# Kernel tuning notes

Measured on AMD Instinct MI355X. Metric: run time of the kernel, lower is better.

The kernel has to match this reference:

```python
import jax, jax.numpy as jnp
import numpy as np

B, N, D, E = 4, 16384, 128, 1048576  # batch, nodes/graph, hidden, total edges


def setup_inputs() -> dict:
    key = jax.random.key(0)
    k0, k1, k2, k3, k4, k5, k6 = jax.random.split(key, 7)
    x = jax.random.normal(k0, (B, N, D), dtype=jnp.float32)
    W = jax.random.normal(k1, (D, D), dtype=jnp.float32) * 0.05  # 'random_normal' init
    b = jax.random.normal(k2, (D,), dtype=jnp.float32) * 0.05
    edge_b = jax.random.randint(k3, (E,), 0, B, dtype=jnp.int32)
    edge_row = jax.random.randint(k4, (E,), 0, N, dtype=jnp.int32)
    edge_col = jax.random.randint(k5, (E,), 0, N, dtype=jnp.int32)
    edge_vals = jax.random.uniform(k6, (E,), dtype=jnp.float32)
    return {"x": x, "W": W, "b": b, "edge_b": edge_b, "edge_row": edge_row,
            "edge_col": edge_col, "edge_vals": edge_vals, "k": 2}


def reference(x, W, b, edge_b, edge_row, edge_col, edge_vals, k):
    # adj is a batched sparse [B, N, N]; edges stored as (batch, row, col, val) COO.
    seg_row = edge_b * N + edge_row  # flattened destination id in [0, B*N)
    # in_degrees = sum_j |adj[b, i, j]|
    deg = jax.ops.segment_sum(jnp.abs(edge_vals), seg_row, num_segments=B * N)
    deg = deg.reshape(B, N)
    norm = jnp.power(deg + 1e-6, -0.5)[..., None]          # [B, N, 1]
    norm_k = jnp.power(norm, k)                             # computed but unused (faithful to source)
    support = jnp.einsum('bnd,de->bne', x, W)               # x @ W
    y = (support * norm).reshape(B * N, D)                  # pre-normalized features
    # SpMM: out[b, i] = sum_{(b,i,j)} adj_val * y[b, j]
    msgs = y[edge_b * N + edge_col] * edge_vals[:, None]    # [E, D] gather + scale
    agg = jax.ops.segment_sum(msgs, seg_row, num_segments=B * N).reshape(B, N, D)
    return jax.nn.relu(agg * norm + b)
```

## Files before the change

kernel.cpp:

```cpp
#include <hip/hip_runtime.h>
#include <stdint.h>

#define B_ 4
#define N_ 16384
#define D_ 128
#define E_ 1048576
#define BN_ 65536
#define NBKT 256
#define NBLK 256
#define CAP  6144

typedef __attribute__((ext_vector_type(8))) short short8;
typedef __attribute__((ext_vector_type(4))) float floatx4;

static constexpr size_t OFF_Y      = 0;
static constexpr size_t OFF_PACK2  = 16777216;
static constexpr size_t OFF_GBKT   = OFF_PACK2 + 12582912;
static constexpr size_t OFF_CURSOR = OFF_GBKT + 1024;
static constexpr size_t OFF_NORM   = OFF_CURSOR + 262144;
static constexpr size_t OFF_WH     = OFF_NORM + 262144;
static constexpr size_t OFF_WL     = OFF_WH + 32768;

__device__ __forceinline__ uint32_t rne16(uint32_t u) {
    return (u + 0x7FFFu + ((u >> 16) & 1u)) >> 16;
}
__device__ __forceinline__ void bf16split(float f, uint16_t& h, uint16_t& l) {
    uint32_t hb = rne16(__float_as_uint(f));
    h = (uint16_t)hb;
    float r = f - __uint_as_float(hb << 16);
    l = (uint16_t)rne16(__float_as_uint(r));
}

__global__ __launch_bounds__(1024) void k_scatter(const int* __restrict__ eb,
                                                  const int* __restrict__ er,
                                                  const int* __restrict__ ec,
                                                  const float* __restrict__ ev,
                                                  const float* __restrict__ Wg,
                                                  uint32_t* __restrict__ gbkt,
                                                  uint2* __restrict__ pack1,
                                                  uint16_t* __restrict__ WhG,
                                                  uint16_t* __restrict__ WlG) {
    __shared__ uint2    ed[4096];
    __shared__ uint32_t h[NBKT];
    int t = threadIdx.x;
    if (t < NBKT) h[t] = 0;
    if (blockIdx.x < 16) {
        int g = blockIdx.x * 1024 + t;
        float w = Wg[g];
        uint16_t hh, ll;
        bf16split(w, hh, ll);
        int k = g >> 7, n = g & 127;
        int o = ((k >> 3) * 128 + n) * 8 + (k & 7);
        WhG[o] = hh;
        WlG[o] = ll;
    }
    __syncthreads();
    int vbase = blockIdx.x * 1024 + t;
    int4   b4 = ((const int4*)eb)[vbase];
    int4   r4 = ((const int4*)er)[vbase];
    int4   c4 = ((const int4*)ec)[vbase];
    float4 v4 = ((const float4*)ev)[vbase];
    uint32_t k0 = (uint32_t)(b4.x * N_ + r4.x);
    uint32_t k1 = (uint32_t)(b4.y * N_ + r4.y);
    uint32_t k2 = (uint32_t)(b4.z * N_ + r4.z);
    uint32_t k3 = (uint32_t)(b4.w * N_ + r4.w);
    ed[t * 4 + 0] = make_uint2((k0 << 14) | (uint32_t)c4.x, __float_as_uint(v4.x));
    ed[t * 4 + 1] = make_uint2((k1 << 14) | (uint32_t)c4.y, __float_as_uint(v4.y));
    ed[t * 4 + 2] = make_uint2((k2 << 14) | (uint32_t)c4.z, __float_as_uint(v4.z));
    ed[t * 4 + 3] = make_uint2((k3 << 14) | (uint32_t)c4.w, __float_as_uint(v4.w));
    atomicAdd(&h[k0 >> 8], 1u);
    atomicAdd(&h[k1 >> 8], 1u);
    atomicAdd(&h[k2 >> 8], 1u);
    atomicAdd(&h[k3 >> 8], 1u);
    __syncthreads();
    if (t < NBKT) {
        uint32_t c = h[t];
        uint32_t base = c ? atomicAdd(&gbkt[t], c) : 0u;
        h[t] = base;
    }
    __syncthreads();
#pragma unroll
    for (int i = 0; i < 4; ++i) {
        uint2 en = ed[t * 4 + i];
        uint32_t bkt = en.x >> 22;
        uint32_t off = atomicAdd(&h[bkt], 1u);
        pack1[(size_t)bkt * CAP + off] = make_uint2(en.x & 0x3FFFFFu, en.y);
    }
}

__global__ __launch_bounds__(1024) void k_build(const uint32_t* __restrict__ gbkt,
                                                const uint2* __restrict__ pack1,
                                                uint2* __restrict__ pack2,
                                                uint32_t* __restrict__ cursor,
                                                float* __restrict__ norm) {
    __shared__ uint32_t cnt[NBKT];
    __shared__ float    dsum[NBKT];
    __shared__ uint32_t scn[NBKT];
    __shared__ uint32_t rcur[NBKT];
    int t = threadIdx.x;
    int bkt = blockIdx.x;
    uint32_t bstart = (uint32_t)bkt * CAP;
    uint32_t bend = bstart + gbkt[bkt];
    if (t < NBKT) { cnt[t] = 0; dsum[t] = 0.f; }
    __syncthreads();
    for (uint32_t i = bstart + t; i < bend; i += 1024) {
        uint2 p = pack1[i];
        uint32_t nl = p.x >> 14;
        atomicAdd(&cnt[nl], 1u);
        atomicAdd(&dsum[nl], fabsf(__uint_as_float(p.y)));
    }
    __syncthreads();
    if (t < NBKT) scn[t] = cnt[t];
    __syncthreads();
    for (int off = 1; off < NBKT; off <<= 1) {
        uint32_t a = 0;
        if (t < NBKT && t >= off) a = scn[t - off];
        __syncthreads();
        if (t < NBKT) scn[t] += a;
        __syncthreads();
    }
    if (t < NBKT) {
        uint32_t incl = scn[t];
        uint32_t excl = incl - cnt[t];
        rcur[t] = bstart + excl;
        cursor[bkt * NBKT + t] = bstart + incl;
        norm[bkt * NBKT + t] = rsqrtf(dsum[t] + 1e-6f);
    }
    __syncthreads();
    uint32_t colbase = (uint32_t)(bkt >> 6) * N_;
    for (uint32_t i = bstart + t; i < bend; i += 1024) {
        uint2 p = pack1[i];
        uint32_t nl = p.x >> 14;
        uint32_t pos = atomicAdd(&rcur[nl], 1u);
        pack2[pos] = make_uint2(colbase + (p.x & 0x3FFFu), p.y);
    }
}

__global__ __launch_bounds__(256) void k_matmul_mfma(const float* __restrict__ x,
                                                     const uint16_t* __restrict__ WhG,
                                                     const uint16_t* __restrict__ WlG,
                                                     const float* __restrict__ norm,
                                                     uint32_t* __restrict__ ybf) {
    __shared__ short WhS[16384];
    __shared__ short WlS[16384];
    __shared__ short XhS[4096];
    __shared__ short XlS[4096];
    __shared__ float normS[32];
    int tid = threadIdx.x;
    int row0 = blockIdx.x * 32;

    {
        const uint4* whg = (const uint4*)WhG;
        const uint4* wlg = (const uint4*)WlG;
        uint4* whs = (uint4*)WhS;
        uint4* wls = (uint4*)WlS;
#pragma unroll
        for (int i = 0; i < 8; ++i) {
            whs[i * 256 + tid] = whg[i * 256 + tid];
            wls[i * 256 + tid] = wlg[i * 256 + tid];
        }
    }
#pragma unroll
    for (int cc = 0; cc < 2; ++cc) {
        int c = cc * 256 + tid;
        int m = c & 31, kk = c >> 5;
        const float4* xp = (const float4*)(x + (size_t)(row0 + m) * D_ + kk * 8);
        float4 f0 = xp[0], f1 = xp[1];
        union { short8 v; uint16_t s[8]; } uh, ul;
        bf16split(f0.x, uh.s[0], ul.s[0]); bf16split(f0.y, uh.s[1], ul.s[1]);
        bf16split(f0.z, uh.s[2], ul.s[2]); bf16split(f0.w, uh.s[3], ul.s[3]);
        bf16split(f1.x, uh.s[4], ul.s[4]); bf16split(f1.y, uh.s[5], ul.s[5]);
        bf16split(f1.z, uh.s[6], ul.s[6]); bf16split(f1.w, uh.s[7], ul.s[7]);
        ((short8*)XhS)[c] = uh.v;
        ((short8*)XlS)[c] = ul.v;
    }
    if (tid < 32) normS[tid] = norm[row0 + tid];
    __syncthreads();

    int lane = tid & 63;
    int wv = tid >> 6;
    int quad = lane >> 4;
    int l15 = lane & 15;
    int wcol0 = wv * 32;
    floatx4 acc[2][2] = {};
    const short8* Xh8 = (const short8*)XhS;
    const short8* Xl8 = (const short8*)XlS;
    const short8* Wh8 = (const short8*)WhS;
    const short8* Wl8 = (const short8*)WlS;
#pragma unroll
    for (int ks = 0; ks < 4; ++ks) {
        int kkq = ks * 4 + quad;
        short8 ah0 = Xh8[kkq * 32 + l15];
        short8 ah1 = Xh8[kkq * 32 + 16 + l15];
        short8 al0 = Xl8[kkq * 32 + l15];
        short8 al1 = Xl8[kkq * 32 + 16 + l15];
        short8 bh0 = Wh8[kkq * 128 + wcol0 + l15];
        short8 bh1 = Wh8[kkq * 128 + wcol0 + 16 + l15];
        short8 bl0 = Wl8[kkq * 128 + wcol0 + l15];
        short8 bl1 = Wl8[kkq * 128 + wcol0 + 16 + l15];
        acc[0][0] = __builtin_amdgcn_mfma_f32_16x16x32_bf16(ah0, bh0, acc[0][0], 0, 0, 0);
        acc[0][1] = __builtin_amdgcn_mfma_f32_16x16x32_bf16(ah0, bh1, acc[0][1], 0, 0, 0);
        acc[1][0] = __builtin_amdgcn_mfma_f32_16x16x32_bf16(ah1, bh0, acc[1][0], 0, 0, 0);
        acc[1][1] = __builtin_amdgcn_mfma_f32_16x16x32_bf16(ah1, bh1, acc[1][1], 0, 0, 0);
        acc[0][0] = __builtin_amdgcn_mfma_f32_16x16x32_bf16(ah0, bl0, acc[0][0], 0, 0, 0);
        acc[0][1] = __builtin_amdgcn_mfma_f32_16x16x32_bf16(ah0, bl1, acc[0][1], 0, 0, 0);
        acc[1][0] = __builtin_amdgcn_mfma_f32_16x16x32_bf16(ah1, bl0, acc[1][0], 0, 0, 0);
        acc[1][1] = __builtin_amdgcn_mfma_f32_16x16x32_bf16(ah1, bl1, acc[1][1], 0, 0, 0);
        acc[0][0] = __builtin_amdgcn_mfma_f32_16x16x32_bf16(al0, bh0, acc[0][0], 0, 0, 0);
        acc[0][1] = __builtin_amdgcn_mfma_f32_16x16x32_bf16(al0, bh1, acc[0][1], 0, 0, 0);
        acc[1][0] = __builtin_amdgcn_mfma_f32_16x16x32_bf16(al1, bh0, acc[1][0], 0, 0, 0);
        acc[1][1] = __builtin_amdgcn_mfma_f32_16x16x32_bf16(al1, bh1, acc[1][1], 0, 0, 0);
    }

#pragma unroll
    for (int rt = 0; rt < 2; ++rt) {
#pragma unroll
        for (int ct = 0; ct < 2; ++ct) {
            floatx4 v = acc[rt][ct];
            int rbase = rt * 16 + quad * 4;
            int cp = (wcol0 + ct * 16) / 2 + (l15 >> 1);
#pragma unroll
            for (int r = 0; r < 4; ++r) {
                float mine = v[r] * normS[rbase + r];
                float oth = __shfl_xor(mine, 1, 64);
                uint32_t a = __float_as_uint((lane & 1) ? oth : mine);
                uint32_t b = __float_as_uint((lane & 1) ? mine : oth);
                uint32_t packed = rne16(a) | (rne16(b) << 16);
                bool doit = ((lane & 1) == 0) ? (r < 2) : (r >= 2);
                if (doit)
                    ybf[(size_t)(row0 + rbase + r) * 64 + cp] = packed;
            }
        }
    }
}

__device__ __forceinline__ void fma8(float* acc, float v, uint4 u) {
    acc[0] = fmaf(v, __uint_as_float(u.x << 16), acc[0]);
    acc[1] = fmaf(v, __uint_as_float(u.x & 0xFFFF0000u), acc[1]);
    acc[2] = fmaf(v, __uint_as_float(u.y << 16), acc[2]);
    acc[3] = fmaf(v, __uint_as_float(u.y & 0xFFFF0000u), acc[3]);
    acc[4] = fmaf(v, __uint_as_float(u.z << 16), acc[4]);
    acc[5] = fmaf(v, __uint_as_float(u.z & 0xFFFF0000u), acc[5]);
    acc[6] = fmaf(v, __uint_as_float(u.w << 16), acc[6]);
    acc[7] = fmaf(v, __uint_as_float(u.w & 0xFFFF0000u), acc[7]);
}

__global__ __launch_bounds__(256) void k_spmm(const uint32_t* __restrict__ cursor,
                                              const uint2* __restrict__ pack,
                                              const uint4* __restrict__ y4,
                                              const float* __restrict__ norm,
                                              const float* __restrict__ bias,
                                              float* __restrict__ out) {
    int blk = blockIdx.x;
    int xcd = blk & 7;
    int j = blk >> 3;
    int nodeblk = (xcd & 3) * 4096 + (xcd >> 2) * 2048 + j;
    int node = nodeblk * 4 + (threadIdx.x >> 6);
    int lane = threadIdx.x & 63;
    int esub = lane >> 4;
    int chunk = lane & 15;
    int nl = node & 255;
    uint32_t end = cursor[node];
    uint32_t start = (nl == 0) ? (uint32_t)(node >> 8) * CAP : cursor[node - 1];
    float acc[8] = {0.f,0.f,0.f,0.f,0.f,0.f,0.f,0.f};
    uint32_t e = start;
    for (; e + 16 <= end; e += 16) {
        uint2 pa = pack[e + 0 + esub];
        uint2 pb = pack[e + 4 + esub];
        uint2 pc = pack[e + 8 + esub];
        uint2 pd = pack[e + 12 + esub];
        uint4 ua = y4[(size_t)pa.x * 16 + chunk];
        uint4 ub = y4[(size_t)pb.x * 16 + chunk];
        uint4 uc = y4[(size_t)pc.x * 16 + chunk];
        uint4 ud = y4[(size_t)pd.x * 16 + chunk];
        fma8(acc, __uint_as_float(pa.y), ua);
        fma8(acc, __uint_as_float(pb.y), ub);
        fma8(acc, __uint_as_float(pc.y), uc);
        fma8(acc, __uint_as_float(pd.y), ud);
    }
    for (; e + 4 <= end; e += 4) {
        uint2 p = pack[e + esub];
        uint4 u = y4[(size_t)p.x * 16 + chunk];
        fma8(acc, __uint_as_float(p.y), u);
    }
    if (e < end) {
        uint32_t idx = e + esub;
        bool act = idx < end;
        uint2 p = pack[act ? idx : (end - 1)];
        uint4 u = y4[(size_t)p.x * 16 + chunk];
        float v = act ? __uint_as_float(p.y) : 0.f;
        fma8(acc, v, u);
    }
#pragma unroll
    for (int i = 0; i < 8; ++i) {
        acc[i] += __shfl_xor(acc[i], 16, 64);
        acc[i] += __shfl_xor(acc[i], 32, 64);
    }
    if (esub < 2) {
        float nm = norm[node];
        float4 bb = ((const float4*)bias)[chunk * 2 + esub];
        float4 o;
        o.x = fmaxf(fmaf(acc[esub * 4 + 0], nm, bb.x), 0.f);
        o.y = fmaxf(fmaf(acc[esub * 4 + 1], nm, bb.y), 0.f);
        o.z = fmaxf(fmaf(acc[esub * 4 + 2], nm, bb.z), 0.f);
        o.w = fmaxf(fmaf(acc[esub * 4 + 3], nm, bb.w), 0.f);
        ((float4*)out)[(size_t)node * 32 + chunk * 2 + esub] = o;
    }
}

extern "C" void kernel_launch(void* const* d_in, const int* in_sizes, int n_in,
                              void* d_out, int out_size, void* d_ws, size_t ws_size,
                              hipStream_t stream) {
    const float* x  = (const float*)d_in[0];
    const float* W  = (const float*)d_in[1];
    const float* bi = (const float*)d_in[2];
    const int* eb   = (const int*)d_in[3];
    const int* er   = (const int*)d_in[4];
    const int* ec   = (const int*)d_in[5];
    const float* ev = (const float*)d_in[6];
    float* out = (float*)d_out;

    char* ws = (char*)d_ws;
    uint32_t* ybf    = (uint32_t*)(ws + OFF_Y);
    uint2*    pack1  = (uint2*)(ws + OFF_Y);
    uint2*    pack2  = (uint2*)(ws + OFF_PACK2);
    uint32_t* gbkt   = (uint32_t*)(ws + OFF_GBKT);
    uint32_t* cursor = (uint32_t*)(ws + OFF_CURSOR);
    float*    norm   = (float*)(ws + OFF_NORM);
    uint16_t* WhG    = (uint16_t*)(ws + OFF_WH);
    uint16_t* WlG    = (uint16_t*)(ws + OFF_WL);

    hipMemsetAsync(gbkt, 0, NBKT * sizeof(uint32_t), stream);
    k_scatter<<<NBLK, 1024, 0, stream>>>(eb, er, ec, ev, W, gbkt, pack1, WhG, WlG);
    k_build  <<<NBKT, 1024, 0, stream>>>(gbkt, pack1, pack2, cursor, norm);
    k_matmul_mfma<<<BN_ / 32, 256, 0, stream>>>(x, WhG, WlG, norm, ybf);
    k_spmm   <<<BN_ / 4, 256, 0, stream>>>(cursor, pack2, (const uint4*)ybf, norm, bi, out);
}
```

Before: 183.7 us.

## Fuse per-bucket row sort into SpMM kernel via shared memory

The row-sorting of edges moves from a separate build kernel into the SpMM kernel. Each 1024-thread block loads one bucket into LDS, counting-sorts it by local row, then has each wave process 16 rows. This removes the global pack2 and cursor arrays and their extra write/read pass. The build kernel shrinks to a degree-only kernel. In exchange, SpMM runs with only 256 large blocks and heavy LDS use, which lowers latency hiding for the random gathers.

```diff
diff --git a/kernel.cpp b/kernel.cpp
--- a/kernel.cpp
+++ b/kernel.cpp
@@ -14,10 +14,9 @@
 typedef __attribute__((ext_vector_type(4))) float floatx4;
 
 static constexpr size_t OFF_Y      = 0;
-static constexpr size_t OFF_PACK2  = 16777216;
-static constexpr size_t OFF_GBKT   = OFF_PACK2 + 12582912;
-static constexpr size_t OFF_CURSOR = OFF_GBKT + 1024;
-static constexpr size_t OFF_NORM   = OFF_CURSOR + 262144;
+static constexpr size_t OFF_PACK1  = 16777216;
+static constexpr size_t OFF_GBKT   = OFF_PACK1 + 12582912;
+static constexpr size_t OFF_NORM   = OFF_GBKT + 1024;
 static constexpr size_t OFF_WH     = OFF_NORM + 262144;
 static constexpr size_t OFF_WL     = OFF_WH + 32768;
 
@@ -88,52 +87,22 @@
     }
 }
 
-__global__ __launch_bounds__(1024) void k_build(const uint32_t* __restrict__ gbkt,
-                                                const uint2* __restrict__ pack1,
-                                                uint2* __restrict__ pack2,
-                                                uint32_t* __restrict__ cursor,
-                                                float* __restrict__ norm) {
-    __shared__ uint32_t cnt[NBKT];
-    __shared__ float    dsum[NBKT];
-    __shared__ uint32_t scn[NBKT];
-    __shared__ uint32_t rcur[NBKT];
+__global__ __launch_bounds__(1024) void k_deg(const uint32_t* __restrict__ gbkt,
+                                              const uint2* __restrict__ pack1,
+                                              float* __restrict__ norm) {
+    __shared__ float dsum[NBKT];
     int t = threadIdx.x;
     int bkt = blockIdx.x;
-    uint32_t bstart = (uint32_t)bkt * CAP;
-    uint32_t bend = bstart + gbkt[bkt];
-    if (t < NBKT) { cnt[t] = 0; dsum[t] = 0.f; }
-    __syncthreads();
-    for (uint32_t i = bstart + t; i < bend; i += 1024) {
-        uint2 p = pack1[i];
-        uint32_t nl = p.x >> 14;
-        atomicAdd(&cnt[nl], 1u);
-        atomicAdd(&dsum[nl], fabsf(__uint_as_float(p.y)));
-    }
-    __syncthreads();
-    if (t < NBKT) scn[t] = cnt[t];
-    __syncthreads();
-    for (int off = 1; off < NBKT; off <<= 1) {
-        uint32_t a = 0;
-        if (t < NBKT && t >= off) a = scn[t - off];
-        __syncthreads();
-        if (t < NBKT) scn[t] += a;
-        __syncthreads();
-    }
-    if (t < NBKT) {
-        uint32_t incl = scn[t];
-        uint32_t excl = incl - cnt[t];
-        rcur[t] = bstart + excl;
-        cursor[bkt * NBKT + t] = bstart + incl;
-        norm[bkt * NBKT + t] = rsqrtf(dsum[t] + 1e-6f);
-    }
-    __syncthreads();
-    uint32_t colbase = (uint32_t)(bkt >> 6) * N_;
-    for (uint32_t i = bstart + t; i < bend; i += 1024) {
-        uint2 p = pack1[i];
-        uint32_t nl = p.x >> 14;
-        uint32_t pos = atomicAdd(&rcur[nl], 1u);
-        pack2[pos] = make_uint2(colbase + (p.x & 0x3FFFu), p.y);
-    }
+    if (t < NBKT) dsum[t] = 0.f;
+    __syncthreads();
+    uint32_t cnt = gbkt[bkt];
+    size_t bstart = (size_t)bkt * CAP;
+    for (uint32_t i = t; i < cnt; i += 1024) {
+        uint2 p = pack1[bstart + i];
+        atomicAdd(&dsum[p.x >> 14], fabsf(__uint_as_float(p.y)));
+    }
+    __syncthreads();
+    if (t < NBKT) norm[bkt * NBKT + t] = rsqrtf(dsum[t] + 1e-6f);
 }
 
 __global__ __launch_bounds__(256) void k_matmul_mfma(const float* __restrict__ x,
@@ -245,66 +214,97 @@
     acc[7] = fmaf(v, __uint_as_float(u.w & 0xFFFF0000u), acc[7]);
 }
 
-__global__ __launch_bounds__(256) void k_spmm(const uint32_t* __restrict__ cursor,
-                                              const uint2* __restrict__ pack,
-                                              const uint4* __restrict__ y4,
-                                              const float* __restrict__ norm,
-                                              const float* __restrict__ bias,
-                                              float* __restrict__ out) {
+__global__ __launch_bounds__(1024) void k_spmm(const uint32_t* __restrict__ gbkt,
+                                               const uint2* __restrict__ pack1,
+                                               const uint4* __restrict__ y4,
+                                               const float* __restrict__ norm,
+                                               const float* __restrict__ bias,
+                                               float* __restrict__ out) {
+    __shared__ uint2    raw[CAP];
+    __shared__ uint2    srt[CAP];
+    __shared__ uint32_t cnt[NBKT];
+    __shared__ uint32_t scn[NBKT];
+    __shared__ uint32_t rcur[NBKT];
+    int t = threadIdx.x;
     int blk = blockIdx.x;
     int xcd = blk & 7;
-    int j = blk >> 3;
-    int nodeblk = (xcd & 3) * 4096 + (xcd >> 2) * 2048 + j;
-    int node = nodeblk * 4 + (threadIdx.x >> 6);
-    int lane = threadIdx.x & 63;
+    int bkt = ((xcd & 3) << 6) | ((xcd >> 2) << 5) | (blk >> 3);
+    if (t < NBKT) cnt[t] = 0;
+    __syncthreads();
+    uint32_t n = gbkt[bkt];
+    size_t base = (size_t)bkt * CAP;
+    for (uint32_t i = t; i < n; i += 1024) {
+        uint2 p = pack1[base + i];
+        raw[i] = p;
+        atomicAdd(&cnt[p.x >> 14], 1u);
+    }
+    __syncthreads();
+    if (t < NBKT) scn[t] = cnt[t];
+    __syncthreads();
+    for (int off = 1; off < NBKT; off <<= 1) {
+        uint32_t a = 0;
+        if (t < NBKT && t >= off) a = scn[t - off];
+        __syncthreads();
+        if (t < NBKT) scn[t] += a;
+        __syncthreads();
+    }
+    if (t < NBKT) rcur[t] = scn[t] - cnt[t];
+    __syncthreads();
+    for (uint32_t i = t; i < n; i += 1024) {
+        uint2 p = raw[i];
+        uint32_t pos = atomicAdd(&rcur[p.x >> 14], 1u);
+        srt[pos] = p;
+    }
+    __syncthreads();
+
+    int wv = t >> 6;
+    int lane = t & 63;
     int esub = lane >> 4;
     int chunk = lane & 15;
-    int nl = node & 255;
-    uint32_t end = cursor[node];
-    uint32_t start = (nl == 0) ? (uint32_t)(node >> 8) * CAP : cursor[node - 1];
-    float acc[8] = {0.f,0.f,0.f,0.f,0.f,0.f,0.f,0.f};
-    uint32_t e = start;
-    for (; e + 16 <= end; e += 16) {
-        uint2 pa = pack[e + 0 + esub];
-        uint2 pb = pack[e + 4 + esub];
-        uint2 pc = pack[e + 8 + esub];
-        uint2 pd = pack[e + 12 + esub];
-        uint4 ua = y4[(size_t)pa.x * 16 + chunk];
-        uint4 ub = y4[(size_t)pb.x * 16 + chunk];
-        uint4 uc = y4[(size_t)pc.x * 16 + chunk];
-        uint4 ud = y4[(size_t)pd.x * 16 + chunk];
-        fma8(acc, __uint_as_float(pa.y), ua);
-        fma8(acc, __uint_as_float(pb.y), ub);
-        fma8(acc, __uint_as_float(pc.y), uc);
-        fma8(acc, __uint_as_float(pd.y), ud);
-    }
-    for (; e + 4 <= end; e += 4) {
-        uint2 p = pack[e + esub];
-        uint4 u = y4[(size_t)p.x * 16 + chunk];
-        fma8(acc, __uint_as_float(p.y), u);
-    }
-    if (e < end) {
-        uint32_t idx = e + esub;
-        bool act = idx < end;
-        uint2 p = pack[act ? idx : (end - 1)];
-        uint4 u = y4[(size_t)p.x * 16 + chunk];
-        float v = act ? __uint_as_float(p.y) : 0.f;
-        fma8(acc, v, u);
-    }
-#pragma unroll
-    for (int i = 0; i < 8; ++i) {
-        acc[i] += __shfl_xor(acc[i], 16, 64);
-        acc[i] += __shfl_xor(acc[i], 32, 64);
-    }
-    if (esub < 2) {
-        float nm = norm[node];
-        float4 bb = ((const float4*)bias)[chunk * 2 + esub];
-        float4 o;
-        o.x = fmaxf(fmaf(acc[esub * 4 + 0], nm, bb.x), 0.f);
-        o.y = fmaxf(fmaf(acc[esub * 4 + 1], nm, bb.y), 0.f);
-        o.z = fmaxf(fmaf(acc[esub * 4 + 2], nm, bb.z), 0.f);
-        o.w = fmaxf(fmaf(acc[esub * 4 + 3], nm, bb.w), 0.f);
-        ((float4*)out)[(size_t)node * 32 + chunk * 2 + esub] = o;
+    uint32_t colbase = (uint32_t)(bkt >> 6) << 14;
+#pragma unroll 1
+    for (int i = 0; i < 16; ++i) {
+        int nl = wv * 16 + i;
+        uint32_t end = scn[nl];
+        uint32_t e = end - cnt[nl];
+        float acc[8] = {0.f,0.f,0.f,0.f,0.f,0.f,0.f,0.f};
+        for (; e + 8 <= end; e += 8) {
+            uint2 p0 = srt[e + esub];
+            uint2 p1 = srt[e + 4 + esub];
+            uint4 u0 = y4[(size_t)(colbase | (p0.x & 0x3FFFu)) * 16 + chunk];
+            uint4 u1 = y4[(size_t)(colbase | (p1.x & 0x3FFFu)) * 16 + chunk];
+            fma8(acc, __uint_as_float(p0.y), u0);
+            fma8(acc, __uint_as_float(p1.y), u1);
+        }
+        for (; e + 4 <= end; e += 4) {
+            uint2 p = srt[e + esub];
+            uint4 u = y4[(size_t)(colbase | (p.x & 0x3FFFu)) * 16 + chunk];
+            fma8(acc, __uint_as_float(p.y), u);
+        }
+        if (e < end) {
+            uint32_t idx = e + esub;
+            bool act = idx < end;
+            uint2 p = srt[act ? idx : (end - 1)];
+            uint4 u = y4[(size_t)(colbase | (p.x & 0x3FFFu)) * 16 + chunk];
+            float v = act ? __uint_as_float(p.y) : 0.f;
+            fma8(acc, v, u);
+        }
+#pragma unroll
+        for (int j = 0; j < 8; ++j) {
+            acc[j] += __shfl_xor(acc[j], 16, 64);
+            acc[j] += __shfl_xor(acc[j], 32, 64);
+        }
+        if (esub < 2) {
+            int node = bkt * NBKT + nl;
+            float nm = norm[node];
+            float4 bb = ((const float4*)bias)[chunk * 2 + esub];
+            float4 o;
+            o.x = fmaxf(fmaf(acc[esub * 4 + 0], nm, bb.x), 0.f);
+            o.y = fmaxf(fmaf(acc[esub * 4 + 1], nm, bb.y), 0.f);
+            o.z = fmaxf(fmaf(acc[esub * 4 + 2], nm, bb.z), 0.f);
+            o.w = fmaxf(fmaf(acc[esub * 4 + 3], nm, bb.w), 0.f);
+            ((float4*)out)[(size_t)node * 32 + chunk * 2 + esub] = o;
+        }
     }
 }
 
@@ -322,17 +322,15 @@
 
     char* ws = (char*)d_ws;
     uint32_t* ybf    = (uint32_t*)(ws + OFF_Y);
-    uint2*    pack1  = (uint2*)(ws + OFF_Y);
-    uint2*    pack2  = (uint2*)(ws + OFF_PACK2);
+    uint2*    pack1  = (uint2*)(ws + OFF_PACK1);
     uint32_t* gbkt   = (uint32_t*)(ws + OFF_GBKT);
-    uint32_t* cursor = (uint32_t*)(ws + OFF_CURSOR);
     float*    norm   = (float*)(ws + OFF_NORM);
     uint16_t* WhG    = (uint16_t*)(ws + OFF_WH);
     uint16_t* WlG    = (uint16_t*)(ws + OFF_WL);
 
     hipMemsetAsync(gbkt, 0, NBKT * sizeof(uint32_t), stream);
     k_scatter<<<NBLK, 1024, 0, stream>>>(eb, er, ec, ev, W, gbkt, pack1, WhG, WlG);
-    k_build  <<<NBKT, 1024, 0, stream>>>(gbkt, pack1, pack2, cursor, norm);
+    k_deg    <<<NBKT, 1024, 0, stream>>>(gbkt, pack1, norm);
     k_matmul_mfma<<<BN_ / 32, 256, 0, stream>>>(x, WhG, WlG, norm, ybf);
-    k_spmm   <<<BN_ / 4, 256, 0, stream>>>(cursor, pack2, (const uint4*)ybf, norm, bi, out);
-}
+    k_spmm   <<<NBKT, 1024, 0, stream>>>(gbkt, pack1, (const uint4*)ybf, norm, bi, out);
+}
```

After: 183.7 us. About the same (-0.0%).
